# Kernel tuning notes

Hardware: AMD Instinct MI355X
Metric: run time of the kernel (lower is better)

The kernel has to match this reference:

```python
import jax, jax.numpy as jnp
import numpy as np

N_NODES = 100000
N_EDGES = 1600000
N_FEAT = 48
N_EDGE_FEAT = 16
HIDDEN = 128


def setup_inputs() -> dict:
    key = jax.random.key(0)
    ks = jax.random.split(key, 8)
    tot = 2 * N_FEAT + N_EDGE_FEAT  # 112
    s1 = 1.0 / np.sqrt(tot)
    s2 = 1.0 / np.sqrt(HIDDEN)
    return {
        "x": jax.random.normal(ks[0], (N_NODES, N_FEAT), dtype=jnp.float32),
        "edge_index": jax.random.randint(ks[1], (2, N_EDGES), 0, N_NODES, dtype=jnp.int64),
        "edge_feat": jax.random.normal(ks[2], (N_EDGES, N_EDGE_FEAT), dtype=jnp.float32),
        "W1": jax.random.normal(ks[3], (tot, HIDDEN), dtype=jnp.float32) * s1,
        "b1": jnp.zeros((HIDDEN,), dtype=jnp.float32),
        "W2": jax.random.normal(ks[4], (HIDDEN, HIDDEN), dtype=jnp.float32) * s2,
        "b2": jnp.zeros((HIDDEN,), dtype=jnp.float32),
        "W3": jax.random.normal(ks[5], (HIDDEN, N_FEAT), dtype=jnp.float32) * s2,
        "b3": jnp.zeros((N_FEAT,), dtype=jnp.float32),
    }


def reference(x, edge_index, edge_feat, W1, b1, W2, b2, W3, b3):
    source = edge_index[0]
    target = edge_index[1]
    # gather + concat: (n_edges, 2*n_feat + n_edge_feat)
    edge = jnp.concatenate([x[source], x[target], edge_feat], axis=-1)
    # 3-layer MLP with ReLU
    h = jax.nn.relu(edge @ W1 + b1)
    h = jax.nn.relu(h @ W2 + b2)
    message = h @ W3 + b3  # (n_edges, n_feat)
    # scatter-mean over target indices
    n = x.shape[0]
    msum = jax.ops.segment_sum(message, target, num_segments=n)
    cnt = jax.ops.segment_sum(jnp.ones((target.shape[0],), dtype=x.dtype), target, num_segments=n)
    update = msum / jnp.maximum(cnt, 1.0)[:, None]  # empty segments -> 0
    return x + update
```

## Files before the change

### kernel.cpp

```cpp
#include <hip/hip_runtime.h>
#include <hip/hip_bf16.h>


#define NN 100000
#define NE 1600000
#define NF 48
#define TOT 112
#define HID 128
#define TILE 256
#define NTILE 6250

typedef __attribute__((ext_vector_type(8))) short short8;
typedef __attribute__((ext_vector_type(4))) float floatx4;

__device__ __forceinline__ unsigned short f2bf(float f) {
    union { float f; unsigned u; } v; v.f = f;
    unsigned u = v.u;
    return (unsigned short)((u + 0x7FFFu + ((u >> 16) & 1u)) >> 16);
}
__device__ __forceinline__ unsigned pack2bf(float a, float b) {
    return (unsigned)f2bf(a) | ((unsigned)f2bf(b) << 16);
}

__global__ void prep_kernel(const float* __restrict__ W1, const float* __restrict__ W2,
                            const float* __restrict__ W3,
                            unsigned short* __restrict__ wt1, unsigned short* __restrict__ wt2,
                            unsigned short* __restrict__ wt3) {
    int idx = blockIdx.x * 256 + threadIdx.x;
    if (idx < 16384) {
        int n = idx >> 7, k = idx & 127;
        wt1[idx] = (k < TOT) ? f2bf(W1[k * HID + n]) : (unsigned short)0;
    } else if (idx < 32768) {
        int j = idx - 16384; int n = j >> 7, k = j & 127;
        wt2[j] = f2bf(W2[k * HID + n]);
    } else if (idx < 38912) {
        int j = idx - 32768; int n = j >> 7, k = j & 127;
        wt3[j] = f2bf(W3[k * NF + n]);
    }
}

__global__ void hist_kernel(const int* __restrict__ ei, int* __restrict__ cnt) {
    int e = blockIdx.x * 256 + threadIdx.x;
    atomicAdd(cnt + ei[NE + e], 1);
}

__global__ void scan_kernel(const int* __restrict__ cnt, int* __restrict__ off,
                            int* __restrict__ counter) {
    __shared__ int sd[256];
    __shared__ int sbase;
    int tid = threadIdx.x;
    int n = blockIdx.x * 256 + tid;
    int v = (n < NN) ? cnt[n] : 0;
    sd[tid] = v;
    __syncthreads();
#pragma unroll
    for (int d = 1; d < 256; d <<= 1) {
        int t = (tid >= d) ? sd[tid - d] : 0;
        __syncthreads();
        sd[tid] += t;
        __syncthreads();
    }
    if (tid == 255) sbase = atomicAdd(counter, sd[255]);
    __syncthreads();
    if (n < NN) off[n] = sbase + sd[tid] - v;
}

__global__ void place_kernel(const int* __restrict__ ei, int* __restrict__ off,
                             int4* __restrict__ srt) {
    int e = blockIdx.x * 256 + threadIdx.x;
    int t = ei[NE + e];
    int p = atomicAdd(off + t, 1);
    srt[p] = make_int4(e, ei[e], t, 0);
}

__device__ __forceinline__ const short8* frag_ptr(const unsigned short* base, int row, int s,
                                                  int lane15, int quad) {
    return (const short8*)((const char*)base + row * 256 + (((s * 4 + quad) ^ lane15) << 4));
}

__launch_bounds__(512, 2)
__global__ void gemm_kernel(const float* __restrict__ x, const float* __restrict__ ef,
                            const int4* __restrict__ srt,
                            const unsigned short* __restrict__ wt1,
                            const unsigned short* __restrict__ wt2,
                            const unsigned short* __restrict__ wt3,
                            const float* __restrict__ b1, const float* __restrict__ b2,
                            float* __restrict__ out_acc) {
    __shared__ __align__(16) unsigned short lw1[128 * 128];
    __shared__ __align__(16) unsigned short lw2[128 * 128];
    __shared__ __align__(16) unsigned short lw3[48 * 128];
    __shared__ __align__(16) unsigned short ea[TILE * 128];
    __shared__ float lb1[128], lb2[128];
    __shared__ int ltgt[TILE];
    __shared__ int seg_start[TILE + 4];
    __shared__ int seg_tgt[TILE];
    __shared__ int nseg;

    const int tid = threadIdx.x;
    const uint4* s1 = (const uint4*)wt1;
    for (int i = tid; i < 2048; i += 512) {
        int n = i >> 4, g = i & 15;
        *(uint4*)((char*)lw1 + n * 256 + ((g ^ (n & 15)) << 4)) = s1[i];
    }
    const uint4* s2 = (const uint4*)wt2;
    for (int i = tid; i < 2048; i += 512) {
        int n = i >> 4, g = i & 15;
        *(uint4*)((char*)lw2 + n * 256 + ((g ^ (n & 15)) << 4)) = s2[i];
    }
    const uint4* s3 = (const uint4*)wt3;
    for (int i = tid; i < 768; i += 512) {
        int n = i >> 4, g = i & 15;
        *(uint4*)((char*)lw3 + n * 256 + ((g ^ (n & 15)) << 4)) = s3[i];
    }
    if (tid < 128) lb1[tid] = b1[tid];
    else if (tid < 256) lb2[tid - 128] = b2[tid - 128];
    __syncthreads();

    const int l15 = tid & 15;
    const int q = (tid & 63) >> 4;
    const int ln = tid & 63;
    const int wave = tid >> 6;
    const int sub = ln & 1;
    const int grow = wave * 32 + (ln >> 1);
    const int gl15 = grow & 15;
    float* lmsg = (float*)ea;

    for (int tile = blockIdx.x; tile < NTILE; tile += gridDim.x) {
        const int e0 = tile * TILE;
        if (tid < TILE) ltgt[tid] = srt[e0 + tid].z;
        {
            int4 es = srt[e0 + grow];
            float4 v[14];
#pragma unroll
            for (int j = 0; j < 14; ++j) {
                int p = 2 * j + sub;
                const float4* gp;
                if (p < 12)      gp = (const float4*)(x + 48 * (size_t)es.y) + p;
                else if (p < 24) gp = (const float4*)(x + 48 * (size_t)es.z) + (p - 12);
                else             gp = (const float4*)(ef + 16 * (size_t)es.x) + (p - 24);
                v[j] = *gp;
            }
#pragma unroll
            for (int j = 0; j < 14; ++j) {
                uint2 h = make_uint2(pack2bf(v[j].x, v[j].y), pack2bf(v[j].z, v[j].w));
                *(uint2*)((char*)ea + grow * 256 + ((j ^ gl15) << 4) + (sub << 3)) = h;
            }
            *(uint4*)((char*)ea + grow * 256 + (((14 + sub) ^ gl15) << 4)) =
                make_uint4(0u, 0u, 0u, 0u);
        }
#pragma unroll
        for (int layer = 0; layer < 2; ++layer) {
            const unsigned short* lw = layer ? lw2 : lw1;
            const float* lb = layer ? lb2 : lb1;
            short8 bf[2][4];
#pragma unroll
            for (int gi = 0; gi < 2; ++gi)
#pragma unroll
                for (int s = 0; s < 4; ++s)
                    bf[gi][s] = *frag_ptr(ea, (wave * 2 + gi) * 16 + l15, s, l15, q);
#pragma unroll
            for (int mt = 0; mt < 8; ++mt) {
                floatx4 a0 = (floatx4){0.f, 0.f, 0.f, 0.f};
                floatx4 a1 = (floatx4){0.f, 0.f, 0.f, 0.f};
#pragma unroll
                for (int s = 0; s < 4; ++s) {
                    short8 a = *frag_ptr(lw, mt * 16 + l15, s, l15, q);
                    a0 = __builtin_amdgcn_mfma_f32_16x16x32_bf16(a, bf[0][s], a0, 0, 0, 0);
                    a1 = __builtin_amdgcn_mfma_f32_16x16x32_bf16(a, bf[1][s], a1, 0, 0, 0);
                }
                int f0 = mt * 16 + q * 4;
                const float4 bv = *(const float4*)(lb + f0);
                uint2 h0 = make_uint2(
                    pack2bf(fmaxf(a0[0] + bv.x, 0.f), fmaxf(a0[1] + bv.y, 0.f)),
                    pack2bf(fmaxf(a0[2] + bv.z, 0.f), fmaxf(a0[3] + bv.w, 0.f)));
                uint2 h1 = make_uint2(
                    pack2bf(fmaxf(a1[0] + bv.x, 0.f), fmaxf(a1[1] + bv.y, 0.f)),
                    pack2bf(fmaxf(a1[2] + bv.z, 0.f), fmaxf(a1[3] + bv.w, 0.f)));
                int gran = 2 * mt + (q >> 1), off8 = (q & 1) << 3;
                *(uint2*)((char*)ea + (wave * 32 + l15) * 256 + ((gran ^ l15) << 4) + off8) = h0;
                *(uint2*)((char*)ea + (wave * 32 + 16 + l15) * 256 + ((gran ^ l15) << 4) + off8) = h1;
            }
        }
        {
            short8 bf[2][4];
#pragma unroll
            for (int gi = 0; gi < 2; ++gi)
#pragma unroll
                for (int s = 0; s < 4; ++s)
                    bf[gi][s] = *frag_ptr(ea, (wave * 2 + gi) * 16 + l15, s, l15, q);
#pragma unroll
            for (int mt = 0; mt < 3; ++mt) {
                floatx4 a0 = (floatx4){0.f, 0.f, 0.f, 0.f};
                floatx4 a1 = (floatx4){0.f, 0.f, 0.f, 0.f};
#pragma unroll
                for (int s = 0; s < 4; ++s) {
                    short8 a = *frag_ptr(lw3, mt * 16 + l15, s, l15, q);
                    a0 = __builtin_amdgcn_mfma_f32_16x16x32_bf16(a, bf[0][s], a0, 0, 0, 0);
                    a1 = __builtin_amdgcn_mfma_f32_16x16x32_bf16(a, bf[1][s], a1, 0, 0, 0);
                }
                int gran = mt * 4 + q;
                *(float4*)((char*)ea + (wave * 32 + l15) * 256 + ((gran ^ l15) << 4)) =
                    *(float4*)&a0;
                *(float4*)((char*)ea + (wave * 32 + 16 + l15) * 256 + ((gran ^ l15) << 4)) =
                    *(float4*)&a1;
            }
        }
        __syncthreads();
        if (wave == 0) {
            int base = 0;
#pragma unroll
            for (int c = 0; c < 4; ++c) {
                int p = c * 64 + ln;
                int t = ltgt[p];
                int flag = (p == 0) || (t != ltgt[p - 1]);
                unsigned long long mask = __ballot(flag);
                int sid = base + __popcll(mask & ((1ull << ln) - 1ull));
                if (flag) { seg_start[sid] = p; seg_tgt[sid] = t; }
                base += __popcll(mask);
            }
            if (ln == 0) { nseg = base; seg_start[base] = TILE; }
        }
        __syncthreads();
        if (ln < 48) {
            const int gcol = ln >> 2, coff = (ln & 3) << 2;
            for (int s = wave; s < nseg; s += 8) {
                int a = seg_start[s], bnd = seg_start[s + 1];
                float s0 = 0.f, s1f = 0.f;
                int p = a;
                for (; p + 1 < bnd; p += 2) {
                    s0  += *(const float*)((const char*)ea + p * 256 +
                                           ((gcol ^ (p & 15)) << 4) + coff);
                    s1f += *(const float*)((const char*)ea + (p + 1) * 256 +
                                           ((gcol ^ ((p + 1) & 15)) << 4) + coff);
                }
                if (p < bnd)
                    s0 += *(const float*)((const char*)ea + p * 256 +
                                          ((gcol ^ (p & 15)) << 4) + coff);
                atomicAdd(out_acc + 48 * (size_t)seg_tgt[s] + ln, s0 + s1f);
            }
        }
        __syncthreads();
    }
}

__global__ void finalize_kernel(const float* __restrict__ x, const int* __restrict__ cnt,
                                const float* __restrict__ b3, float* __restrict__ out) {
    int i = blockIdx.x * 256 + threadIdx.x;
    float c = (float)cnt[i / 48];
    float upd = (c > 0.f) ? (out[i] / c + b3[i % 48]) : 0.f;
    out[i] = x[i] + upd;
}

extern "C" void kernel_launch(void* const* d_in, const int* in_sizes, int n_in,
                              void* d_out, int out_size, void* d_ws, size_t ws_size,
                              hipStream_t stream) {
    const float* x  = (const float*)d_in[0];
    const int*   ei = (const int*)d_in[1];
    const float* ef = (const float*)d_in[2];
    const float* W1 = (const float*)d_in[3];
    const float* b1 = (const float*)d_in[4];
    const float* W2 = (const float*)d_in[5];
    const float* b2 = (const float*)d_in[6];
    const float* W3 = (const float*)d_in[7];
    const float* b3 = (const float*)d_in[8];
    float* out = (float*)d_out;

    char* ws = (char*)d_ws;
    int* cnt     = (int*)ws;
    int* off     = (int*)(ws + 409600);
    int* counter = (int*)(ws + 819200);
    unsigned short* wt1 = (unsigned short*)(ws + 819456);
    unsigned short* wt2 = wt1 + 16384;
    unsigned short* wt3 = wt2 + 16384;
    int4* srt = (int4*)(ws + 901120);

    hipMemsetAsync(out, 0, (size_t)out_size * sizeof(float), stream);
    hipMemsetAsync(cnt, 0, (size_t)NN * sizeof(int), stream);
    hipMemsetAsync(counter, 0, sizeof(int), stream);
    prep_kernel<<<152, 256, 0, stream>>>(W1, W2, W3, wt1, wt2, wt3);
    hist_kernel<<<6250, 256, 0, stream>>>(ei, cnt);
    scan_kernel<<<391, 256, 0, stream>>>(cnt, off, counter);
    place_kernel<<<6250, 256, 0, stream>>>(ei, off, srt);
    gemm_kernel<<<256, 512, 0, stream>>>(x, ef, srt, wt1, wt2, wt3, b1, b2, out);
    finalize_kernel<<<NN * NF / 256, 256, 0, stream>>>(x, cnt, b3, out);
}
```

Measured before the change: 615.7 us.

## Make edge tiles wave-independent and pack sorted edge records into 64 bits

Each wave now processes its own 32-edge chunk end to end. Segment boundaries come from a shuffle plus ballot rather than a block-level scan in shared memory, which removes the two __syncthreads per tile and the serial wave-0 segmentation step. Sorted edge records shrink from int4 to a packed 64-bit word, halving that traffic in place and gemm. Float-to-bf16 packing uses the HIP intrinsic. Smaller segments may produce more atomics per node, because segments that cross a 32-edge boundary get split.

```diff
diff --git a/kernel.cpp b/kernel.cpp
--- a/kernel.cpp
+++ b/kernel.cpp
@@ -7,8 +7,7 @@
 #define NF 48
 #define TOT 112
 #define HID 128
-#define TILE 256
-#define NTILE 6250
+#define NCHUNK 50000
 
 typedef __attribute__((ext_vector_type(8))) short short8;
 typedef __attribute__((ext_vector_type(4))) float floatx4;
@@ -18,8 +17,9 @@
     unsigned u = v.u;
     return (unsigned short)((u + 0x7FFFu + ((u >> 16) & 1u)) >> 16);
 }
-__device__ __forceinline__ unsigned pack2bf(float a, float b) {
-    return (unsigned)f2bf(a) | ((unsigned)f2bf(b) << 16);
+__device__ __forceinline__ unsigned pk2(float a, float b) {
+    __hip_bfloat162 h = __float22bfloat162_rn(make_float2(a, b));
+    return *(unsigned*)&h;
 }
 
 __global__ void prep_kernel(const float* __restrict__ W1, const float* __restrict__ W2,
@@ -66,11 +66,12 @@
 }
 
 __global__ void place_kernel(const int* __restrict__ ei, int* __restrict__ off,
-                             int4* __restrict__ srt) {
+                             unsigned long long* __restrict__ srt) {
     int e = blockIdx.x * 256 + threadIdx.x;
     int t = ei[NE + e];
     int p = atomicAdd(off + t, 1);
-    srt[p] = make_int4(e, ei[e], t, 0);
+    srt[p] = (unsigned long long)e | ((unsigned long long)ei[e] << 21) |
+             ((unsigned long long)t << 38);
 }
 
 __device__ __forceinline__ const short8* frag_ptr(const unsigned short* base, int row, int s,
@@ -80,7 +81,7 @@
 
 __launch_bounds__(512, 2)
 __global__ void gemm_kernel(const float* __restrict__ x, const float* __restrict__ ef,
-                            const int4* __restrict__ srt,
+                            const unsigned long long* __restrict__ srt,
                             const unsigned short* __restrict__ wt1,
                             const unsigned short* __restrict__ wt2,
                             const unsigned short* __restrict__ wt3,
@@ -89,12 +90,8 @@
     __shared__ __align__(16) unsigned short lw1[128 * 128];
     __shared__ __align__(16) unsigned short lw2[128 * 128];
     __shared__ __align__(16) unsigned short lw3[48 * 128];
-    __shared__ __align__(16) unsigned short ea[TILE * 128];
+    __shared__ __align__(16) unsigned short ea[256 * 128];
     __shared__ float lb1[128], lb2[128];
-    __shared__ int ltgt[TILE];
-    __shared__ int seg_start[TILE + 4];
-    __shared__ int seg_tgt[TILE];
-    __shared__ int nseg;
 
     const int tid = threadIdx.x;
     const uint4* s1 = (const uint4*)wt1;
@@ -121,33 +118,40 @@
     const int ln = tid & 63;
     const int wave = tid >> 6;
     const int sub = ln & 1;
-    const int grow = wave * 32 + (ln >> 1);
+    const int row = ln >> 1;
+    const int grow = wave * 32 + row;
     const int gl15 = grow & 15;
-    float* lmsg = (float*)ea;
-
-    for (int tile = blockIdx.x; tile < NTILE; tile += gridDim.x) {
-        const int e0 = tile * TILE;
-        if (tid < TILE) ltgt[tid] = srt[e0 + tid].z;
+    const int gwid = blockIdx.x * 8 + wave;
+    const int gtot = gridDim.x * 8;
+
+    for (int c = gwid; c < NCHUNK; c += gtot) {
+        const int e0 = c * 32;
+        unsigned long long pk = srt[e0 + row];
+        int eid = (int)(pk & 0x1FFFFFull);
+        int src = (int)((pk >> 21) & 0x1FFFFull);
+        int tgt = (int)(pk >> 38);
         {
-            int4 es = srt[e0 + grow];
             float4 v[14];
 #pragma unroll
             for (int j = 0; j < 14; ++j) {
                 int p = 2 * j + sub;
                 const float4* gp;
-                if (p < 12)      gp = (const float4*)(x + 48 * (size_t)es.y) + p;
-                else if (p < 24) gp = (const float4*)(x + 48 * (size_t)es.z) + (p - 12);
-                else             gp = (const float4*)(ef + 16 * (size_t)es.x) + (p - 24);
+                if (p < 12)      gp = (const float4*)(x + 48 * (size_t)src) + p;
+                else if (p < 24) gp = (const float4*)(x + 48 * (size_t)tgt) + (p - 12);
+                else             gp = (const float4*)(ef + 16 * (size_t)eid) + (p - 24);
                 v[j] = *gp;
             }
 #pragma unroll
             for (int j = 0; j < 14; ++j) {
-                uint2 h = make_uint2(pack2bf(v[j].x, v[j].y), pack2bf(v[j].z, v[j].w));
+                uint2 h = make_uint2(pk2(v[j].x, v[j].y), pk2(v[j].z, v[j].w));
                 *(uint2*)((char*)ea + grow * 256 + ((j ^ gl15) << 4) + (sub << 3)) = h;
             }
             *(uint4*)((char*)ea + grow * 256 + (((14 + sub) ^ gl15) << 4)) =
                 make_uint4(0u, 0u, 0u, 0u);
         }
+        int tprev = __shfl_up(tgt, 2);
+        int flag = (row == 0) || (tgt != tprev);
+        unsigned long long bmask = __ballot(sub == 0 && flag);
 #pragma unroll
         for (int layer = 0; layer < 2; ++layer) {
             const unsigned short* lw = layer ? lw2 : lw1;
@@ -170,12 +174,10 @@
                 }
                 int f0 = mt * 16 + q * 4;
                 const float4 bv = *(const float4*)(lb + f0);
-                uint2 h0 = make_uint2(
-                    pack2bf(fmaxf(a0[0] + bv.x, 0.f), fmaxf(a0[1] + bv.y, 0.f)),
-                    pack2bf(fmaxf(a0[2] + bv.z, 0.f), fmaxf(a0[3] + bv.w, 0.f)));
-                uint2 h1 = make_uint2(
-                    pack2bf(fmaxf(a1[0] + bv.x, 0.f), fmaxf(a1[1] + bv.y, 0.f)),
-                    pack2bf(fmaxf(a1[2] + bv.z, 0.f), fmaxf(a1[3] + bv.w, 0.f)));
+                uint2 h0 = make_uint2(pk2(fmaxf(a0[0] + bv.x, 0.f), fmaxf(a0[1] + bv.y, 0.f)),
+                                      pk2(fmaxf(a0[2] + bv.z, 0.f), fmaxf(a0[3] + bv.w, 0.f)));
+                uint2 h1 = make_uint2(pk2(fmaxf(a1[0] + bv.x, 0.f), fmaxf(a1[1] + bv.y, 0.f)),
+                                      pk2(fmaxf(a1[2] + bv.z, 0.f), fmaxf(a1[3] + bv.w, 0.f)));
                 int gran = 2 * mt + (q >> 1), off8 = (q & 1) << 3;
                 *(uint2*)((char*)ea + (wave * 32 + l15) * 256 + ((gran ^ l15) << 4) + off8) = h0;
                 *(uint2*)((char*)ea + (wave * 32 + 16 + l15) * 256 + ((gran ^ l15) << 4) + off8) = h1;
@@ -205,41 +207,26 @@
                     *(float4*)&a1;
             }
         }
-        __syncthreads();
-        if (wave == 0) {
-            int base = 0;
-#pragma unroll
-            for (int c = 0; c < 4; ++c) {
-                int p = c * 64 + ln;
-                int t = ltgt[p];
-                int flag = (p == 0) || (t != ltgt[p - 1]);
-                unsigned long long mask = __ballot(flag);
-                int sid = base + __popcll(mask & ((1ull << ln) - 1ull));
-                if (flag) { seg_start[sid] = p; seg_tgt[sid] = t; }
-                base += __popcll(mask);
-            }
-            if (ln == 0) { nseg = base; seg_start[base] = TILE; }
-        }
-        __syncthreads();
-        if (ln < 48) {
+        {
+            unsigned long long m = bmask;
+            int nseg = __popcll(m);
             const int gcol = ln >> 2, coff = (ln & 3) << 2;
-            for (int s = wave; s < nseg; s += 8) {
-                int a = seg_start[s], bnd = seg_start[s + 1];
-                float s0 = 0.f, s1f = 0.f;
-                int p = a;
-                for (; p + 1 < bnd; p += 2) {
-                    s0  += *(const float*)((const char*)ea + p * 256 +
-                                           ((gcol ^ (p & 15)) << 4) + coff);
-                    s1f += *(const float*)((const char*)ea + (p + 1) * 256 +
-                                           ((gcol ^ ((p + 1) & 15)) << 4) + coff);
+            for (int s = 0; s < nseg; ++s) {
+                int b = __builtin_ctzll(m); m &= m - 1;
+                int start = b >> 1;
+                int end = m ? (__builtin_ctzll(m) >> 1) : 32;
+                int t = __shfl(tgt, b);
+                if (ln < 48) {
+                    float acc = 0.f;
+                    for (int r = start; r < end; ++r) {
+                        int rr = wave * 32 + r;
+                        acc += *(const float*)((const char*)ea + rr * 256 +
+                                               ((gcol ^ (rr & 15)) << 4) + coff);
+                    }
+                    atomicAdd(out_acc + 48 * (size_t)t + ln, acc);
                 }
-                if (p < bnd)
-                    s0 += *(const float*)((const char*)ea + p * 256 +
-                                          ((gcol ^ (p & 15)) << 4) + coff);
-                atomicAdd(out_acc + 48 * (size_t)seg_tgt[s] + ln, s0 + s1f);
-            }
-        }
-        __syncthreads();
+            }
+        }
     }
 }
 
@@ -272,7 +259,7 @@
     unsigned short* wt1 = (unsigned short*)(ws + 819456);
     unsigned short* wt2 = wt1 + 16384;
     unsigned short* wt3 = wt2 + 16384;
-    int4* srt = (int4*)(ws + 901120);
+    unsigned long long* srt = (unsigned long long*)(ws + 901120);
 
     hipMemsetAsync(out, 0, (size_t)out_size * sizeof(float), stream);
     hipMemsetAsync(cnt, 0, (size_t)NN * sizeof(int), stream);
```

New measurement: 959.1 us. +55.8%, slower.
